# Performance work log

Measured on AMD Instinct MI355X. Metric: run time of the kernel, lower is better.

The kernel has to match this reference:

```python
import jax, jax.numpy as jnp
import numpy as np

N_NODES = 100000
N_EDGES = 1600000
D = 128


def _gconv(x, edge_index, edge_weight, W, Wloop, b):
    # support = x @ W ; out = adj @ support + x @ Wloop + b
    support = x @ W                                   # [N, D]
    src, dst = edge_index[0], edge_index[1]
    msgs = support[src] * edge_weight[:, None]        # [E, D] gather (irregular)
    agg = jax.ops.segment_sum(msgs, dst, num_segments=x.shape[0])  # [N, D] scatter
    return agg + x @ Wloop + b


def setup_inputs() -> dict:
    key = jax.random.key(0)
    ks = jax.random.split(key, 9)
    s = 1.0 / np.sqrt(D)
    x = jax.random.normal(ks[0], (N_NODES, D), dtype=jnp.float32)
    edge_index = jax.random.randint(ks[1], (2, N_EDGES), 0, N_NODES, dtype=jnp.int32)
    edge_weight = jax.random.uniform(ks[2], (N_EDGES,), dtype=jnp.float32)
    W1 = jax.random.normal(ks[3], (D, D), dtype=jnp.float32) * s
    Wloop1 = jax.random.normal(ks[4], (D, D), dtype=jnp.float32) * s
    b1 = jax.random.normal(ks[5], (D,), dtype=jnp.float32) * 0.01
    W2 = jax.random.normal(ks[6], (D, D), dtype=jnp.float32) * s
    Wloop2 = jax.random.normal(ks[7], (D, D), dtype=jnp.float32) * s
    b2 = jax.random.normal(ks[8], (D,), dtype=jnp.float32) * 0.01
    return {"x": x, "edge_index": edge_index, "edge_weight": edge_weight,
            "W1": W1, "Wloop1": Wloop1, "b1": b1,
            "W2": W2, "Wloop2": Wloop2, "b2": b2}


def reference(x, edge_index, edge_weight, W1, Wloop1, b1, W2, Wloop2, b2):
    h = _gconv(x, edge_index, edge_weight, W1, Wloop1, b1)
    h = _gconv(h, edge_index, edge_weight, W2, Wloop2, b2)
    return (x + h) * 0.5
```

## Files before the change

### kernel.cpp

```cpp
#include <hip/hip_runtime.h>
#include <hip/hip_bf16.h>
#include <stdint.h>

#define D 128
#define BM 64
#define NB_BITS 9
#define NPB (1 << NB_BITS)
#define BCAP 10240
#define C3_EPB 4096

typedef __attribute__((ext_vector_type(8))) short bf16x8;
typedef __attribute__((ext_vector_type(4))) short short4_t;
typedef __attribute__((ext_vector_type(4))) float f32x4;
typedef unsigned int uint32;

static __device__ __forceinline__ short f2bf(float f) {
  uint32_t u = __builtin_bit_cast(uint32_t, f);
  u += 0x7fffu + ((u >> 16) & 1u);
  return (short)(u >> 16);
}

static __device__ __forceinline__ uint32 pk2bf(float a, float b) {
  return ((uint32)(unsigned short)f2bf(b) << 16) | (uint32)(unsigned short)f2bf(a);
}


__global__ void k_prep(const float* __restrict__ W1, const float* __restrict__ Wl1,
                       const float* __restrict__ W2, const float* __restrict__ Wl2,
                       short* __restrict__ BT1, short* __restrict__ BT2,
                       int* __restrict__ bcur) {
  int idx = blockIdx.x * 256 + threadIdx.x;
  if (idx < 2 * D * D) {
    int n = idx >> 7, k = idx & (D - 1);
    float v = (n < D) ? W1[k * D + n] : Wl1[k * D + (n - D)];
    BT1[idx] = f2bf(v);
  } else if (idx < 4 * D * D) {
    int i2 = idx - 2 * D * D;
    int n = i2 >> 8, k = i2 & 255;
    float v = (k < D) ? W2[k * D + n] : Wl2[(k - D) * D + n];
    BT2[i2] = f2bf(v);
  } else if (idx < 4 * D * D + 256) {
    bcur[idx - 4 * D * D] = 0;
  }
}


__global__ __launch_bounds__(256) void k_bucket(const int* __restrict__ src,
                                                const int* __restrict__ dst,
                                                const float* __restrict__ wgt,
                                                int* __restrict__ bcur,
                                                int4* __restrict__ rec,
                                                int E, int nb) {
  __shared__ int lhist[256];
  __shared__ int lbase[256];
  const int t = threadIdx.x;
  const int e0 = blockIdx.x * C3_EPB;
  if (t < nb) lhist[t] = 0;
  __syncthreads();
  for (int i = t; i < C3_EPB; i += 256) {
    int e = e0 + i;
    if (e < E) atomicAdd(&lhist[dst[e] >> NB_BITS], 1);
  }
  __syncthreads();
  if (t < nb) {
    lbase[t] = atomicAdd(&bcur[t], lhist[t]);
    lhist[t] = 0;
  }
  __syncthreads();
  for (int i = t; i < C3_EPB; i += 256) {
    int e = e0 + i;
    if (e < E) {
      int d = dst[e];
      int b = d >> NB_BITS;
      int r = lbase[b] + atomicAdd(&lhist[b], 1);
      if (r >= BCAP) r = BCAP - 1;
      rec[(size_t)b * BCAP + r] =
          make_int4(src[e], __builtin_bit_cast(int, wgt[e]), d, 0);
    }
  }
}


__global__ __launch_bounds__(256) void k_sort(const int4* __restrict__ rec,
                                              const int* __restrict__ bcur,
                                              int* __restrict__ off,
                                              int2* __restrict__ pairs,
                                              int N, int nb) {
  __shared__ int bc[256];
  __shared__ int psum[256];
  __shared__ int lofs[NPB];
  const int t = threadIdx.x;
  const int b = blockIdx.x;

  int mycnt = (t < nb) ? min(bcur[t], BCAP) : 0;
  bc[t] = mycnt;
  __syncthreads();
  for (int dd = 1; dd < 256; dd <<= 1) {
    int a = (t >= dd) ? bc[t - dd] : 0;
    __syncthreads();
    bc[t] += a;
    __syncthreads();
  }
  const int cntb = min(bcur[b], BCAP);
  const int ebase = bc[b] - cntb;
  const int total = bc[nb - 1];
  const size_t rbase = (size_t)b * BCAP;
  const int n0 = b << NB_BITS;
  const int nn = min(NPB, N - n0);

  for (int i = t; i < NPB; i += 256) lofs[i] = 0;
  __syncthreads();
  for (int i = t; i < cntb; i += 256)
    atomicAdd(&lofs[rec[rbase + i].z & (NPB - 1)], 1);
  __syncthreads();

  int v0 = lofs[2 * t], v1 = lofs[2 * t + 1];
  int sum = v0 + v1;
  psum[t] = sum;
  __syncthreads();
  for (int dd = 1; dd < 256; dd <<= 1) {
    int a = (t >= dd) ? psum[t - dd] : 0;
    __syncthreads();
    psum[t] += a;
    __syncthreads();
  }
  int run = psum[t] - sum;
  lofs[2 * t] = run;
  lofs[2 * t + 1] = run + v0;
  __syncthreads();

  for (int i = t; i < nn; i += 256) off[n0 + i] = ebase + lofs[i];
  if (b == nb - 1 && t == 0) off[N] = total;
  __syncthreads();

  for (int i = t; i < cntb; i += 256) {
    int4 rr = rec[rbase + i];
    int r = atomicAdd(&lofs[rr.z & (NPB - 1)], 1);
    pairs[ebase + r] = make_int2(rr.x, rr.y);
  }
}


__global__ __launch_bounds__(256) void k_gemm1(const float* __restrict__ A,
                                               const short* __restrict__ BT,
                                               const float* __restrict__ bias,
                                               unsigned short* __restrict__ support,
                                               unsigned short* __restrict__ initp, int M) {
  __shared__ short As[BM * D];
  const int t = threadIdx.x;
  const int l = t & 63;
  const int w = t >> 6;
  const int lm = l & 15;
  const int lg = l >> 4;
  const int m0 = blockIdx.x * BM;
  const bool full = (m0 + BM <= M);

  float4 aregf[8];
#pragma unroll
  for (int i = 0; i < 8; ++i) {
    int id = t + i * 256;
    int row = id >> 5, c4 = id & 31;
    int gr = m0 + row; if (gr >= M) gr = M - 1;
    aregf[i] = *(const float4*)(A + (size_t)gr * D + c4 * 4);
  }

  bf16x8 bfrag[4][4];
  const int colbase = w * 64 + lm;
#pragma unroll
  for (int cf = 0; cf < 4; ++cf) {
    const short* p = BT + (colbase + cf * 16) * D + lg * 8;
#pragma unroll
    for (int ks = 0; ks < 4; ++ks) bfrag[cf][ks] = *(const bf16x8*)(p + ks * 32);
  }

#pragma unroll
  for (int i = 0; i < 8; ++i) {
    int id = t + i * 256;
    int row = id >> 5, c4 = id & 31;
    float4 v = aregf[i];
    short4_t s4 = { f2bf(v.x), f2bf(v.y), f2bf(v.z), f2bf(v.w) };
    int sidx = row * D + ((c4 * 4) ^ ((row & 7) << 3));
    *(short4_t*)(As + sidx) = s4;
  }
  __syncthreads();

  f32x4 acc[4][4] = {};
#pragma unroll
  for (int ks = 0; ks < 4; ++ks) {
    bf16x8 afrag[4];
    int kcol = ks * 32 + lg * 8;
#pragma unroll
    for (int rf = 0; rf < 4; ++rf) {
      int row = rf * 16 + lm;
      afrag[rf] = *(const bf16x8*)(As + row * D + (kcol ^ ((row & 7) << 3)));
    }
#pragma unroll
    for (int rf = 0; rf < 4; ++rf)
#pragma unroll
      for (int cf = 0; cf < 4; ++cf)
        acc[rf][cf] = __builtin_amdgcn_mfma_f32_16x16x32_bf16(
            bfrag[cf][ks], afrag[rf], acc[rf][cf], 0, 0, 0);
  }

  const bool isInit = (w >= 2);
  const int wcol = (w & 1) * 64;

  if (!isInit) {
#pragma unroll
    for (int rf = 0; rf < 4; ++rf) {
      int m = m0 + rf * 16 + lm;
#pragma unroll
      for (int cf = 0; cf < 4; ++cf) {
        int nb = wcol + cf * 16 + lg * 4;
        f32x4 a = acc[rf][cf];
        uint2 pk = make_uint2(pk2bf(a[0], a[1]), pk2bf(a[2], a[3]));
        if (full || m < M)
          *(uint2*)((uint32*)support + (size_t)m * 64 + (nb >> 1)) = pk;
      }
    }
  } else {
    float4 bv4[4];
#pragma unroll
    for (int cf = 0; cf < 4; ++cf)
      bv4[cf] = *(const float4*)(bias + wcol + cf * 16 + lg * 4);
#pragma unroll
    for (int rf = 0; rf < 4; ++rf) {
      int m = m0 + rf * 16 + lm;
      bool ok = full || m < M;
#pragma unroll
      for (int cf = 0; cf < 4; ++cf) {
        int nb = wcol + cf * 16 + lg * 4;
        f32x4 a = acc[rf][cf];
        if (ok) {
          uint2 pk = make_uint2(pk2bf(a[0] + bv4[cf].x, a[1] + bv4[cf].y),
                                pk2bf(a[2] + bv4[cf].z, a[3] + bv4[cf].w));
          *(uint2*)((uint32*)initp + (size_t)m * 64 + (nb >> 1)) = pk;
        }
      }
    }
  }
}


__global__ __launch_bounds__(256) void k_gemm2(const uint32* __restrict__ aggb,
                                               const uint32* __restrict__ h1b,
                                               const short* __restrict__ BT,
                                               const float* __restrict__ bias,
                                               const float* __restrict__ resid,
                                               float* __restrict__ out, int M) {
  __shared__ short As[BM * 256];
  const int t = threadIdx.x;
  const int l = t & 63;
  const int w = t >> 6;
  const int lm = l & 15;
  const int lg = l >> 4;
  const int m0 = blockIdx.x * BM;
  const bool full = (m0 + BM <= M);

#pragma unroll
  for (int i = 0; i < 8; ++i) {
    int id = t + i * 256;
    int row = id >> 5, c8 = id & 31;
    int gr = m0 + row; if (gr >= M) gr = M - 1;
    const uint32* srcp = (c8 < 16) ? (aggb + (size_t)gr * 64 + c8 * 4)
                                   : (h1b + (size_t)gr * 64 + (c8 - 16) * 4);
    uint4 v = *(const uint4*)srcp;
    int sidx = row * 256 + ((c8 * 8) ^ ((row & 7) << 3));
    *(uint4*)(As + sidx) = v;
  }

  bf16x8 bfrag[2][8];
  const int colbase = w * 32 + lm;
#pragma unroll
  for (int cf = 0; cf < 2; ++cf) {
    const short* p = BT + (colbase + cf * 16) * 256 + lg * 8;
#pragma unroll
    for (int ks = 0; ks < 8; ++ks) bfrag[cf][ks] = *(const bf16x8*)(p + ks * 32);
  }
  __syncthreads();

  f32x4 acc[4][2] = {};
#pragma unroll
  for (int ks = 0; ks < 8; ++ks) {
    bf16x8 afrag[4];
    int kcol = ks * 32 + lg * 8;
#pragma unroll
    for (int rf = 0; rf < 4; ++rf) {
      int row = rf * 16 + lm;
      afrag[rf] = *(const bf16x8*)(As + row * 256 + (kcol ^ ((row & 7) << 3)));
    }
#pragma unroll
    for (int rf = 0; rf < 4; ++rf)
#pragma unroll
      for (int cf = 0; cf < 2; ++cf)
        acc[rf][cf] = __builtin_amdgcn_mfma_f32_16x16x32_bf16(
            bfrag[cf][ks], afrag[rf], acc[rf][cf], 0, 0, 0);
  }

  float4 bv4[2];
#pragma unroll
  for (int cf = 0; cf < 2; ++cf)
    bv4[cf] = *(const float4*)(bias + w * 32 + cf * 16 + lg * 4);
#pragma unroll
  for (int rf = 0; rf < 4; ++rf) {
    int m = m0 + rf * 16 + lm;
    bool ok = full || m < M;
    if (!ok) continue;
#pragma unroll
    for (int cf = 0; cf < 2; ++cf) {
      int nb = w * 32 + cf * 16 + lg * 4;
      f32x4 a = acc[rf][cf];
      float4 xr = *(const float4*)(resid + (size_t)m * D + nb);
      float4 v;
      v.x = (a[0] + bv4[cf].x + xr.x) * 0.5f;
      v.y = (a[1] + bv4[cf].y + xr.y) * 0.5f;
      v.z = (a[2] + bv4[cf].z + xr.z) * 0.5f;
      v.w = (a[3] + bv4[cf].w + xr.w) * 0.5f;
      *(float4*)(out + (size_t)m * D + nb) = v;
    }
  }
}


template<int MODE>
__global__ __launch_bounds__(256) void k_agg(const uint32* __restrict__ sup,
                                             const int* __restrict__ off,
                                             const int2* __restrict__ pairs,
                                             uint32* __restrict__ iop, int N) {
  int node = blockIdx.x * 4 + (threadIdx.x >> 6);
  if (node >= N) return;
  const int l = threadIdx.x & 63;
  const int beg = __builtin_amdgcn_readfirstlane(off[node]);
  const int end = __builtin_amdgcn_readfirstlane(off[node + 1]);
  float ax = 0.f, ay = 0.f;
  const int nbt = (end - beg + 7) >> 3;

  if (nbt > 0) {
    int pr[8], pw[8];
#pragma unroll
    for (int i = 0; i < 8; ++i) {
      int jj = beg + i;
      int jc = jj < end ? jj : beg;
      int2 tt = pairs[jc];
      pr[i] = __builtin_amdgcn_readfirstlane(tt.x);
      pw[i] = __builtin_amdgcn_readfirstlane(jj < end ? tt.y : 0);
    }
    int j = beg + 8;
    for (int b = 1; b < nbt; ++b, j += 8) {
      int nr[8], nw[8];
#pragma unroll
      for (int i = 0; i < 8; ++i) {
        int jj = j + i;
        int jc = jj < end ? jj : beg;
        int2 tt = pairs[jc];
        nr[i] = __builtin_amdgcn_readfirstlane(tt.x);
        nw[i] = __builtin_amdgcn_readfirstlane(jj < end ? tt.y : 0);
      }
      uint32 v[8];
#pragma unroll
      for (int i = 0; i < 8; ++i) v[i] = sup[(size_t)(uint32)pr[i] * 64 + l];
#pragma unroll
      for (int i = 0; i < 8; ++i) {
        float w = __builtin_bit_cast(float, pw[i]);
        ax = fmaf(__builtin_bit_cast(float, v[i] << 16), w, ax);
        ay = fmaf(__builtin_bit_cast(float, v[i] & 0xffff0000u), w, ay);
      }
#pragma unroll
      for (int i = 0; i < 8; ++i) { pr[i] = nr[i]; pw[i] = nw[i]; }
    }
    uint32 v[8];
#pragma unroll
    for (int i = 0; i < 8; ++i) v[i] = sup[(size_t)(uint32)pr[i] * 64 + l];
#pragma unroll
    for (int i = 0; i < 8; ++i) {
      float w = __builtin_bit_cast(float, pw[i]);
      ax = fmaf(__builtin_bit_cast(float, v[i] << 16), w, ax);
      ay = fmaf(__builtin_bit_cast(float, v[i] & 0xffff0000u), w, ay);
    }
  }

  size_t o = (size_t)node * 64 + l;
  if (MODE == 0) {
    uint32 cur = iop[o];
    float vx = __builtin_bit_cast(float, cur << 16) + ax;
    float vy = __builtin_bit_cast(float, cur & 0xffff0000u) + ay;
    iop[o] = pk2bf(vx, vy);
  } else {
    iop[o] = pk2bf(ax, ay);
  }
}


extern "C" void kernel_launch(void* const* d_in, const int* in_sizes, int n_in,
                              void* d_out, int out_size, void* d_ws, size_t ws_size,
                              hipStream_t stream) {
  const float* x   = (const float*)d_in[0];
  const int*   ei  = (const int*)d_in[1];
  const float* ew  = (const float*)d_in[2];
  const float* W1  = (const float*)d_in[3];
  const float* Wl1 = (const float*)d_in[4];
  const float* b1  = (const float*)d_in[5];
  const float* W2  = (const float*)d_in[6];
  const float* Wl2 = (const float*)d_in[7];
  const float* b2  = (const float*)d_in[8];
  float* out = (float*)d_out;

  const int N = in_sizes[0] / D;
  const int E = in_sizes[1] / 2;
  const int* src = ei;
  const int* dst = ei + E;
  const int nbuck = (N + NPB - 1) >> NB_BITS;

  uint32* sup = (uint32*)d_ws;
  uint32* h1b = sup + (size_t)N * 64;
  short* BT1  = (short*)(h1b + (size_t)N * 64);
  short* BT2  = BT1 + 2 * D * D;
  int* bcur   = (int*)(BT2 + 2 * D * D);
  int* off    = bcur + 256;
  int2* pairs = (int2*)(off + (N + 4));
  int4* rec   = (int4*)(pairs + E);
  uint32* aggb = (uint32*)rec;

  k_prep<<<(4 * D * D + 256 + 255) / 256, 256, 0, stream>>>(W1, Wl1, W2, Wl2, BT1, BT2, bcur);

  k_bucket<<<(E + C3_EPB - 1) / C3_EPB, 256, 0, stream>>>(src, dst, ew, bcur, rec, E, nbuck);
  k_sort<<<nbuck, 256, 0, stream>>>(rec, bcur, off, pairs, N, nbuck);

  const int mblocks = (N + BM - 1) / BM;
  const int ablocks = (N + 3) / 4;

  k_gemm1<<<mblocks, 256, 0, stream>>>(x, BT1, b1, (unsigned short*)sup, (unsigned short*)h1b, N);
  k_agg<0><<<ablocks, 256, 0, stream>>>(sup, off, pairs, h1b, N);

  k_agg<2><<<ablocks, 256, 0, stream>>>(h1b, off, pairs, aggb, N);
  k_gemm2<<<mblocks, 256, 0, stream>>>(aggb, h1b, BT2, b2, x, out, N);
}
```

Measured before the change: 249.8 us.

## Fuse second-layer aggregation into the final GEMM kernel

The second gather/segment-sum is moved into the final GEMM kernel. Each wave aggregates 16 node rows into shared memory as bf16, and the h1 tile is loaded into a padded LDS buffer; the MFMA then reads both halves. This removes one kernel launch and the global write and re-read of the intermediate aggregate. In exchange, each block now aggregates its 64 rows with only 4 waves in sequence, so there is less parallelism to hide the latency of irregular gathers than in the separate 4-nodes-per-block kernel.

```diff
diff --git a/kernel.cpp b/kernel.cpp
--- a/kernel.cpp
+++ b/kernel.cpp
@@ -8,6 +8,7 @@
 #define NPB (1 << NB_BITS)
 #define BCAP 10240
 #define C3_EPB 4096
+#define LROW 136
 
 typedef __attribute__((ext_vector_type(8))) short bf16x8;
 typedef __attribute__((ext_vector_type(4))) short short4_t;
@@ -242,87 +243,6 @@
 }
 
 
-__global__ __launch_bounds__(256) void k_gemm2(const uint32* __restrict__ aggb,
-                                               const uint32* __restrict__ h1b,
-                                               const short* __restrict__ BT,
-                                               const float* __restrict__ bias,
-                                               const float* __restrict__ resid,
-                                               float* __restrict__ out, int M) {
-  __shared__ short As[BM * 256];
-  const int t = threadIdx.x;
-  const int l = t & 63;
-  const int w = t >> 6;
-  const int lm = l & 15;
-  const int lg = l >> 4;
-  const int m0 = blockIdx.x * BM;
-  const bool full = (m0 + BM <= M);
-
-#pragma unroll
-  for (int i = 0; i < 8; ++i) {
-    int id = t + i * 256;
-    int row = id >> 5, c8 = id & 31;
-    int gr = m0 + row; if (gr >= M) gr = M - 1;
-    const uint32* srcp = (c8 < 16) ? (aggb + (size_t)gr * 64 + c8 * 4)
-                                   : (h1b + (size_t)gr * 64 + (c8 - 16) * 4);
-    uint4 v = *(const uint4*)srcp;
-    int sidx = row * 256 + ((c8 * 8) ^ ((row & 7) << 3));
-    *(uint4*)(As + sidx) = v;
-  }
-
-  bf16x8 bfrag[2][8];
-  const int colbase = w * 32 + lm;
-#pragma unroll
-  for (int cf = 0; cf < 2; ++cf) {
-    const short* p = BT + (colbase + cf * 16) * 256 + lg * 8;
-#pragma unroll
-    for (int ks = 0; ks < 8; ++ks) bfrag[cf][ks] = *(const bf16x8*)(p + ks * 32);
-  }
-  __syncthreads();
-
-  f32x4 acc[4][2] = {};
-#pragma unroll
-  for (int ks = 0; ks < 8; ++ks) {
-    bf16x8 afrag[4];
-    int kcol = ks * 32 + lg * 8;
-#pragma unroll
-    for (int rf = 0; rf < 4; ++rf) {
-      int row = rf * 16 + lm;
-      afrag[rf] = *(const bf16x8*)(As + row * 256 + (kcol ^ ((row & 7) << 3)));
-    }
-#pragma unroll
-    for (int rf = 0; rf < 4; ++rf)
-#pragma unroll
-      for (int cf = 0; cf < 2; ++cf)
-        acc[rf][cf] = __builtin_amdgcn_mfma_f32_16x16x32_bf16(
-            bfrag[cf][ks], afrag[rf], acc[rf][cf], 0, 0, 0);
-  }
-
-  float4 bv4[2];
-#pragma unroll
-  for (int cf = 0; cf < 2; ++cf)
-    bv4[cf] = *(const float4*)(bias + w * 32 + cf * 16 + lg * 4);
-#pragma unroll
-  for (int rf = 0; rf < 4; ++rf) {
-    int m = m0 + rf * 16 + lm;
-    bool ok = full || m < M;
-    if (!ok) continue;
-#pragma unroll
-    for (int cf = 0; cf < 2; ++cf) {
-      int nb = w * 32 + cf * 16 + lg * 4;
-      f32x4 a = acc[rf][cf];
-      float4 xr = *(const float4*)(resid + (size_t)m * D + nb);
-      float4 v;
-      v.x = (a[0] + bv4[cf].x + xr.x) * 0.5f;
-      v.y = (a[1] + bv4[cf].y + xr.y) * 0.5f;
-      v.z = (a[2] + bv4[cf].z + xr.z) * 0.5f;
-      v.w = (a[3] + bv4[cf].w + xr.w) * 0.5f;
-      *(float4*)(out + (size_t)m * D + nb) = v;
-    }
-  }
-}
-
-
-template<int MODE>
 __global__ __launch_bounds__(256) void k_agg(const uint32* __restrict__ sup,
                                              const int* __restrict__ off,
                                              const int2* __restrict__ pairs,
@@ -380,13 +300,145 @@
   }
 
   size_t o = (size_t)node * 64 + l;
-  if (MODE == 0) {
-    uint32 cur = iop[o];
-    float vx = __builtin_bit_cast(float, cur << 16) + ax;
-    float vy = __builtin_bit_cast(float, cur & 0xffff0000u) + ay;
-    iop[o] = pk2bf(vx, vy);
-  } else {
-    iop[o] = pk2bf(ax, ay);
+  uint32 cur = iop[o];
+  float vx = __builtin_bit_cast(float, cur << 16) + ax;
+  float vy = __builtin_bit_cast(float, cur & 0xffff0000u) + ay;
+  iop[o] = pk2bf(vx, vy);
+}
+
+
+__global__ __launch_bounds__(256) void k_gemm2f(const uint32* __restrict__ h1b,
+                                                const short* __restrict__ BT,
+                                                const float* __restrict__ bias,
+                                                const float* __restrict__ resid,
+                                                const int* __restrict__ off,
+                                                const int2* __restrict__ pairs,
+                                                float* __restrict__ out, int M) {
+  __shared__ short Ag[BM * LROW];
+  __shared__ short Hh[BM * LROW];
+  const int t = threadIdx.x;
+  const int l = t & 63;
+  const int w = t >> 6;
+  const int lm = l & 15;
+  const int lg = l >> 4;
+  const int m0 = blockIdx.x * BM;
+  const bool full = (m0 + BM <= M);
+
+#pragma unroll
+  for (int i = 0; i < 4; ++i) {
+    int id = t + i * 256;
+    int row = id >> 4, c8 = id & 15;
+    int gr = m0 + row; if (gr >= M) gr = M - 1;
+    uint4 v = *(const uint4*)(h1b + (size_t)gr * 64 + c8 * 4);
+    *(uint4*)(Hh + row * LROW + c8 * 8) = v;
+  }
+
+  for (int r = 0; r < 16; ++r) {
+    const int row = w * 16 + r;
+    const int node = m0 + row;
+    float ax = 0.f, ay = 0.f;
+    if (node < M) {
+      const int beg = __builtin_amdgcn_readfirstlane(off[node]);
+      const int end = __builtin_amdgcn_readfirstlane(off[node + 1]);
+      const int nbt = (end - beg + 7) >> 3;
+      if (nbt > 0) {
+        int pr[8], pw[8];
+#pragma unroll
+        for (int i = 0; i < 8; ++i) {
+          int jj = beg + i;
+          int jc = jj < end ? jj : beg;
+          int2 tt = pairs[jc];
+          pr[i] = __builtin_amdgcn_readfirstlane(tt.x);
+          pw[i] = __builtin_amdgcn_readfirstlane(jj < end ? tt.y : 0);
+        }
+        int j = beg + 8;
+        for (int b = 1; b < nbt; ++b, j += 8) {
+          int nr[8], nw[8];
+#pragma unroll
+          for (int i = 0; i < 8; ++i) {
+            int jj = j + i;
+            int jc = jj < end ? jj : beg;
+            int2 tt = pairs[jc];
+            nr[i] = __builtin_amdgcn_readfirstlane(tt.x);
+            nw[i] = __builtin_amdgcn_readfirstlane(jj < end ? tt.y : 0);
+          }
+          uint32 v[8];
+#pragma unroll
+          for (int i = 0; i < 8; ++i) v[i] = h1b[(size_t)(uint32)pr[i] * 64 + l];
+#pragma unroll
+          for (int i = 0; i < 8; ++i) {
+            float wt = __builtin_bit_cast(float, pw[i]);
+            ax = fmaf(__builtin_bit_cast(float, v[i] << 16), wt, ax);
+            ay = fmaf(__builtin_bit_cast(float, v[i] & 0xffff0000u), wt, ay);
+          }
+#pragma unroll
+          for (int i = 0; i < 8; ++i) { pr[i] = nr[i]; pw[i] = nw[i]; }
+        }
+        uint32 v[8];
+#pragma unroll
+        for (int i = 0; i < 8; ++i) v[i] = h1b[(size_t)(uint32)pr[i] * 64 + l];
+#pragma unroll
+        for (int i = 0; i < 8; ++i) {
+          float wt = __builtin_bit_cast(float, pw[i]);
+          ax = fmaf(__builtin_bit_cast(float, v[i] << 16), wt, ax);
+          ay = fmaf(__builtin_bit_cast(float, v[i] & 0xffff0000u), wt, ay);
+        }
+      }
+    }
+    *(uint32*)(Ag + row * LROW + 2 * l) = pk2bf(ax, ay);
+  }
+  __syncthreads();
+
+  bf16x8 bfrag[2][8];
+  const int colbase = w * 32 + lm;
+#pragma unroll
+  for (int cf = 0; cf < 2; ++cf) {
+    const short* p = BT + (colbase + cf * 16) * 256 + lg * 8;
+#pragma unroll
+    for (int ks = 0; ks < 8; ++ks) bfrag[cf][ks] = *(const bf16x8*)(p + ks * 32);
+  }
+
+  f32x4 acc[4][2] = {};
+#pragma unroll
+  for (int ks = 0; ks < 8; ++ks) {
+    bf16x8 afrag[4];
+    int kcol = ks * 32 + lg * 8;
+#pragma unroll
+    for (int rf = 0; rf < 4; ++rf) {
+      int row = rf * 16 + lm;
+      afrag[rf] = (ks < 4)
+          ? *(const bf16x8*)(Ag + row * LROW + kcol)
+          : *(const bf16x8*)(Hh + row * LROW + (kcol - 128));
+    }
+#pragma unroll
+    for (int rf = 0; rf < 4; ++rf)
+#pragma unroll
+      for (int cf = 0; cf < 2; ++cf)
+        acc[rf][cf] = __builtin_amdgcn_mfma_f32_16x16x32_bf16(
+            bfrag[cf][ks], afrag[rf], acc[rf][cf], 0, 0, 0);
+  }
+
+  float4 bv4[2];
+#pragma unroll
+  for (int cf = 0; cf < 2; ++cf)
+    bv4[cf] = *(const float4*)(bias + w * 32 + cf * 16 + lg * 4);
+#pragma unroll
+  for (int rf = 0; rf < 4; ++rf) {
+    int m = m0 + rf * 16 + lm;
+    bool ok = full || m < M;
+    if (!ok) continue;
+#pragma unroll
+    for (int cf = 0; cf < 2; ++cf) {
+      int nb = w * 32 + cf * 16 + lg * 4;
+      f32x4 a = acc[rf][cf];
+      float4 xr = *(const float4*)(resid + (size_t)m * D + nb);
+      float4 v;
+      v.x = (a[0] + bv4[cf].x + xr.x) * 0.5f;
+      v.y = (a[1] + bv4[cf].y + xr.y) * 0.5f;
+      v.z = (a[2] + bv4[cf].z + xr.z) * 0.5f;
+      v.w = (a[3] + bv4[cf].w + xr.w) * 0.5f;
+      *(float4*)(out + (size_t)m * D + nb) = v;
+    }
   }
 }
 
@@ -419,7 +471,6 @@
   int* off    = bcur + 256;
   int2* pairs = (int2*)(off + (N + 4));
   int4* rec   = (int4*)(pairs + E);
-  uint32* aggb = (uint32*)rec;
 
   k_prep<<<(4 * D * D + 256 + 255) / 256, 256, 0, stream>>>(W1, Wl1, W2, Wl2, BT1, BT2, bcur);
 
@@ -430,8 +481,7 @@
   const int ablocks = (N + 3) / 4;
 
   k_gemm1<<<mblocks, 256, 0, stream>>>(x, BT1, b1, (unsigned short*)sup, (unsigned short*)h1b, N);
-  k_agg<0><<<ablocks, 256, 0, stream>>>(sup, off, pairs, h1b, N);
-
-  k_agg<2><<<ablocks, 256, 0, stream>>>(h1b, off, pairs, aggb, N);
-  k_gemm2<<<mblocks, 256, 0, stream>>>(aggb, h1b, BT2, b2, x, out, N);
-}
+  k_agg<<<ablocks, 256, 0, stream>>>(sup, off, pairs, h1b, N);
+
+  k_gemm2f<<<mblocks, 256, 0, stream>>>(h1b, BT2, b2, x, off, pairs, out, N);
+}
```

New measurement: 270.7 us. 1.08x slower.

## Merge edge bucketing and first GEMM into one heterogeneous launch

Applied to the files above, without the earlier changes.

Bucketing of edges and the first dense GEMM were two separate launches. They are now one kernel: block indices below bblocks do the bucketing and the rest do GEMM tiles, sharing a raw shared-memory buffer. This removes a launch and the serialisation between two independent stages, so the memory-bound bucketing and the compute-bound GEMM can overlap on the GPU. k_sort now runs after the combined kernel, and the aggregation kernel definition moves earlier in the file. The cost is that bucketing blocks reserve the GEMM-sized shared allocation, which may limit occupancy.

```diff
diff --git a/kernel.cpp b/kernel.cpp
--- a/kernel.cpp
+++ b/kernel.cpp
@@ -45,37 +45,140 @@
 }
 
 
-__global__ __launch_bounds__(256) void k_bucket(const int* __restrict__ src,
-                                                const int* __restrict__ dst,
-                                                const float* __restrict__ wgt,
-                                                int* __restrict__ bcur,
-                                                int4* __restrict__ rec,
-                                                int E, int nb) {
-  __shared__ int lhist[256];
-  __shared__ int lbase[256];
+__global__ __launch_bounds__(256) void k_b1(const int* __restrict__ src,
+                                            const int* __restrict__ dst,
+                                            const float* __restrict__ wgt,
+                                            int* __restrict__ bcur,
+                                            int4* __restrict__ rec,
+                                            int E, int nb, int bblocks,
+                                            const float* __restrict__ A,
+                                            const short* __restrict__ BT,
+                                            const float* __restrict__ bias,
+                                            unsigned short* __restrict__ support,
+                                            unsigned short* __restrict__ initp, int M) {
+  __shared__ char smraw[BM * D * 2];
   const int t = threadIdx.x;
-  const int e0 = blockIdx.x * C3_EPB;
-  if (t < nb) lhist[t] = 0;
-  __syncthreads();
-  for (int i = t; i < C3_EPB; i += 256) {
-    int e = e0 + i;
-    if (e < E) atomicAdd(&lhist[dst[e] >> NB_BITS], 1);
-  }
-  __syncthreads();
-  if (t < nb) {
-    lbase[t] = atomicAdd(&bcur[t], lhist[t]);
-    lhist[t] = 0;
-  }
-  __syncthreads();
-  for (int i = t; i < C3_EPB; i += 256) {
-    int e = e0 + i;
-    if (e < E) {
-      int d = dst[e];
-      int b = d >> NB_BITS;
-      int r = lbase[b] + atomicAdd(&lhist[b], 1);
-      if (r >= BCAP) r = BCAP - 1;
-      rec[(size_t)b * BCAP + r] =
-          make_int4(src[e], __builtin_bit_cast(int, wgt[e]), d, 0);
+
+  if (blockIdx.x < bblocks) {
+    int* lhist = (int*)smraw;
+    int* lbase = lhist + 256;
+    const int e0 = blockIdx.x * C3_EPB;
+    if (t < nb) lhist[t] = 0;
+    __syncthreads();
+    for (int i = t; i < C3_EPB; i += 256) {
+      int e = e0 + i;
+      if (e < E) atomicAdd(&lhist[dst[e] >> NB_BITS], 1);
+    }
+    __syncthreads();
+    if (t < nb) {
+      lbase[t] = atomicAdd(&bcur[t], lhist[t]);
+      lhist[t] = 0;
+    }
+    __syncthreads();
+    for (int i = t; i < C3_EPB; i += 256) {
+      int e = e0 + i;
+      if (e < E) {
+        int d = dst[e];
+        int b = d >> NB_BITS;
+        int r = lbase[b] + atomicAdd(&lhist[b], 1);
+        if (r >= BCAP) r = BCAP - 1;
+        rec[(size_t)b * BCAP + r] =
+            make_int4(src[e], __builtin_bit_cast(int, wgt[e]), d, 0);
+      }
+    }
+    return;
+  }
+
+  short* As = (short*)smraw;
+  const int l = t & 63;
+  const int w = t >> 6;
+  const int lm = l & 15;
+  const int lg = l >> 4;
+  const int m0 = (blockIdx.x - bblocks) * BM;
+  const bool full = (m0 + BM <= M);
+
+  float4 aregf[8];
+#pragma unroll
+  for (int i = 0; i < 8; ++i) {
+    int id = t + i * 256;
+    int row = id >> 5, c4 = id & 31;
+    int gr = m0 + row; if (gr >= M) gr = M - 1;
+    aregf[i] = *(const float4*)(A + (size_t)gr * D + c4 * 4);
+  }
+
+  bf16x8 bfrag[4][4];
+  const int colbase = w * 64 + lm;
+#pragma unroll
+  for (int cf = 0; cf < 4; ++cf) {
+    const short* p = BT + (colbase + cf * 16) * D + lg * 8;
+#pragma unroll
+    for (int ks = 0; ks < 4; ++ks) bfrag[cf][ks] = *(const bf16x8*)(p + ks * 32);
+  }
+
+#pragma unroll
+  for (int i = 0; i < 8; ++i) {
+    int id = t + i * 256;
+    int row = id >> 5, c4 = id & 31;
+    float4 v = aregf[i];
+    short4_t s4 = { f2bf(v.x), f2bf(v.y), f2bf(v.z), f2bf(v.w) };
+    int sidx = row * D + ((c4 * 4) ^ ((row & 7) << 3));
+    *(short4_t*)(As + sidx) = s4;
+  }
+  __syncthreads();
+
+  f32x4 acc[4][4] = {};
+#pragma unroll
+  for (int ks = 0; ks < 4; ++ks) {
+    bf16x8 afrag[4];
+    int kcol = ks * 32 + lg * 8;
+#pragma unroll
+    for (int rf = 0; rf < 4; ++rf) {
+      int row = rf * 16 + lm;
+      afrag[rf] = *(const bf16x8*)(As + row * D + (kcol ^ ((row & 7) << 3)));
+    }
+#pragma unroll
+    for (int rf = 0; rf < 4; ++rf)
+#pragma unroll
+      for (int cf = 0; cf < 4; ++cf)
+        acc[rf][cf] = __builtin_amdgcn_mfma_f32_16x16x32_bf16(
+            bfrag[cf][ks], afrag[rf], acc[rf][cf], 0, 0, 0);
+  }
+
+  const bool isInit = (w >= 2);
+  const int wcol = (w & 1) * 64;
+
+  if (!isInit) {
+#pragma unroll
+    for (int rf = 0; rf < 4; ++rf) {
+      int m = m0 + rf * 16 + lm;
+#pragma unroll
+      for (int cf = 0; cf < 4; ++cf) {
+        int nb2 = wcol + cf * 16 + lg * 4;
+        f32x4 a = acc[rf][cf];
+        uint2 pk = make_uint2(pk2bf(a[0], a[1]), pk2bf(a[2], a[3]));
+        if (full || m < M)
+          *(uint2*)((uint32*)support + (size_t)m * 64 + (nb2 >> 1)) = pk;
+      }
+    }
+  } else {
+    float4 bv4[4];
+#pragma unroll
+    for (int cf = 0; cf < 4; ++cf)
+      bv4[cf] = *(const float4*)(bias + wcol + cf * 16 + lg * 4);
+#pragma unroll
+    for (int rf = 0; rf < 4; ++rf) {
+      int m = m0 + rf * 16 + lm;
+      bool ok = full || m < M;
+#pragma unroll
+      for (int cf = 0; cf < 4; ++cf) {
+        int nb2 = wcol + cf * 16 + lg * 4;
+        f32x4 a = acc[rf][cf];
+        if (ok) {
+          uint2 pk = make_uint2(pk2bf(a[0] + bv4[cf].x, a[1] + bv4[cf].y),
+                                pk2bf(a[2] + bv4[cf].z, a[3] + bv4[cf].w));
+          *(uint2*)((uint32*)initp + (size_t)m * 64 + (nb2 >> 1)) = pk;
+        }
+      }
     }
   }
 }
@@ -141,103 +244,71 @@
 }
 
 
-__global__ __launch_bounds__(256) void k_gemm1(const float* __restrict__ A,
-                                               const short* __restrict__ BT,
-                                               const float* __restrict__ bias,
-                                               unsigned short* __restrict__ support,
-                                               unsigned short* __restrict__ initp, int M) {
-  __shared__ short As[BM * D];
-  const int t = threadIdx.x;
-  const int l = t & 63;
-  const int w = t >> 6;
-  const int lm = l & 15;
-  const int lg = l >> 4;
-  const int m0 = blockIdx.x * BM;
-  const bool full = (m0 + BM <= M);
-
-  float4 aregf[8];
-#pragma unroll
-  for (int i = 0; i < 8; ++i) {
-    int id = t + i * 256;
-    int row = id >> 5, c4 = id & 31;
-    int gr = m0 + row; if (gr >= M) gr = M - 1;
-    aregf[i] = *(const float4*)(A + (size_t)gr * D + c4 * 4);
-  }
-
-  bf16x8 bfrag[4][4];
-  const int colbase = w * 64 + lm;
-#pragma unroll
-  for (int cf = 0; cf < 4; ++cf) {
-    const short* p = BT + (colbase + cf * 16) * D + lg * 8;
-#pragma unroll
-    for (int ks = 0; ks < 4; ++ks) bfrag[cf][ks] = *(const bf16x8*)(p + ks * 32);
-  }
-
-#pragma unroll
-  for (int i = 0; i < 8; ++i) {
-    int id = t + i * 256;
-    int row = id >> 5, c4 = id & 31;
-    float4 v = aregf[i];
-    short4_t s4 = { f2bf(v.x), f2bf(v.y), f2bf(v.z), f2bf(v.w) };
-    int sidx = row * D + ((c4 * 4) ^ ((row & 7) << 3));
-    *(short4_t*)(As + sidx) = s4;
-  }
-  __syncthreads();
-
-  f32x4 acc[4][4] = {};
-#pragma unroll
-  for (int ks = 0; ks < 4; ++ks) {
-    bf16x8 afrag[4];
-    int kcol = ks * 32 + lg * 8;
-#pragma unroll
-    for (int rf = 0; rf < 4; ++rf) {
-      int row = rf * 16 + lm;
-      afrag[rf] = *(const bf16x8*)(As + row * D + (kcol ^ ((row & 7) << 3)));
-    }
-#pragma unroll
-    for (int rf = 0; rf < 4; ++rf)
-#pragma unroll
-      for (int cf = 0; cf < 4; ++cf)
-        acc[rf][cf] = __builtin_amdgcn_mfma_f32_16x16x32_bf16(
-            bfrag[cf][ks], afrag[rf], acc[rf][cf], 0, 0, 0);
-  }
-
-  const bool isInit = (w >= 2);
-  const int wcol = (w & 1) * 64;
-
-  if (!isInit) {
-#pragma unroll
-    for (int rf = 0; rf < 4; ++rf) {
-      int m = m0 + rf * 16 + lm;
-#pragma unroll
-      for (int cf = 0; cf < 4; ++cf) {
-        int nb = wcol + cf * 16 + lg * 4;
-        f32x4 a = acc[rf][cf];
-        uint2 pk = make_uint2(pk2bf(a[0], a[1]), pk2bf(a[2], a[3]));
-        if (full || m < M)
-          *(uint2*)((uint32*)support + (size_t)m * 64 + (nb >> 1)) = pk;
+template<int MODE>
+__global__ __launch_bounds__(256) void k_agg(const uint32* __restrict__ sup,
+                                             const int* __restrict__ off,
+                                             const int2* __restrict__ pairs,
+                                             uint32* __restrict__ iop, int N) {
+  int node = blockIdx.x * 4 + (threadIdx.x >> 6);
+  if (node >= N) return;
+  const int l = threadIdx.x & 63;
+  const int beg = __builtin_amdgcn_readfirstlane(off[node]);
+  const int end = __builtin_amdgcn_readfirstlane(off[node + 1]);
+  float ax = 0.f, ay = 0.f;
+  const int nbt = (end - beg + 7) >> 3;
+
+  if (nbt > 0) {
+    int pr[8], pw[8];
+#pragma unroll
+    for (int i = 0; i < 8; ++i) {
+      int jj = beg + i;
+      int jc = jj < end ? jj : beg;
+      int2 tt = pairs[jc];
+      pr[i] = __builtin_amdgcn_readfirstlane(tt.x);
+      pw[i] = __builtin_amdgcn_readfirstlane(jj < end ? tt.y : 0);
+    }
+    int j = beg + 8;
+    for (int b = 1; b < nbt; ++b, j += 8) {
+      int nr[8], nw[8];
+#pragma unroll
+      for (int i = 0; i < 8; ++i) {
+        int jj = j + i;
+        int jc = jj < end ? jj : beg;
+        int2 tt = pairs[jc];
+        nr[i] = __builtin_amdgcn_readfirstlane(tt.x);
+        nw[i] = __builtin_amdgcn_readfirstlane(jj < end ? tt.y : 0);
       }
-    }
+      uint32 v[8];
+#pragma unroll
+      for (int i = 0; i < 8; ++i) v[i] = sup[(size_t)(uint32)pr[i] * 64 + l];
+#pragma unroll
+      for (int i = 0; i < 8; ++i) {
+        float w = __builtin_bit_cast(float, pw[i]);
+        ax = fmaf(__builtin_bit_cast(float, v[i] << 16), w, ax);
+        ay = fmaf(__builtin_bit_cast(float, v[i] & 0xffff0000u), w, ay);
+      }
+#pragma unroll
+      for (int i = 0; i < 8; ++i) { pr[i] = nr[i]; pw[i] = nw[i]; }
+    }
+    uint32 v[8];
+#pragma unroll
+    for (int i = 0; i < 8; ++i) v[i] = sup[(size_t)(uint32)pr[i] * 64 + l];
+#pragma unroll
+    for (int i = 0; i < 8; ++i) {
+      float w = __builtin_bit_cast(float, pw[i]);
+      ax = fmaf(__builtin_bit_cast(float, v[i] << 16), w, ax);
+      ay = fmaf(__builtin_bit_cast(float, v[i] & 0xffff0000u), w, ay);
+    }
+  }
+
+  size_t o = (size_t)node * 64 + l;
+  if (MODE == 0) {
+    uint32 cur = iop[o];
+    float vx = __builtin_bit_cast(float, cur << 16) + ax;
+    float vy = __builtin_bit_cast(float, cur & 0xffff0000u) + ay;
+    iop[o] = pk2bf(vx, vy);
   } else {
-    float4 bv4[4];
-#pragma unroll
-    for (int cf = 0; cf < 4; ++cf)
-      bv4[cf] = *(const float4*)(bias + wcol + cf * 16 + lg * 4);
-#pragma unroll
-    for (int rf = 0; rf < 4; ++rf) {
-      int m = m0 + rf * 16 + lm;
-      bool ok = full || m < M;
-#pragma unroll
-      for (int cf = 0; cf < 4; ++cf) {
-        int nb = wcol + cf * 16 + lg * 4;
-        f32x4 a = acc[rf][cf];
-        if (ok) {
-          uint2 pk = make_uint2(pk2bf(a[0] + bv4[cf].x, a[1] + bv4[cf].y),
-                                pk2bf(a[2] + bv4[cf].z, a[3] + bv4[cf].w));
-          *(uint2*)((uint32*)initp + (size_t)m * 64 + (nb >> 1)) = pk;
-        }
-      }
-    }
+    iop[o] = pk2bf(ax, ay);
   }
 }
 
@@ -322,75 +393,6 @@
 }
 
 
-template<int MODE>
-__global__ __launch_bounds__(256) void k_agg(const uint32* __restrict__ sup,
-                                             const int* __restrict__ off,
-                                             const int2* __restrict__ pairs,
-                                             uint32* __restrict__ iop, int N) {
-  int node = blockIdx.x * 4 + (threadIdx.x >> 6);
-  if (node >= N) return;
-  const int l = threadIdx.x & 63;
-  const int beg = __builtin_amdgcn_readfirstlane(off[node]);
-  const int end = __builtin_amdgcn_readfirstlane(off[node + 1]);
-  float ax = 0.f, ay = 0.f;
-  const int nbt = (end - beg + 7) >> 3;
-
-  if (nbt > 0) {
-    int pr[8], pw[8];
-#pragma unroll
-    for (int i = 0; i < 8; ++i) {
-      int jj = beg + i;
-      int jc = jj < end ? jj : beg;
-      int2 tt = pairs[jc];
-      pr[i] = __builtin_amdgcn_readfirstlane(tt.x);
-      pw[i] = __builtin_amdgcn_readfirstlane(jj < end ? tt.y : 0);
-    }
-    int j = beg + 8;
-    for (int b = 1; b < nbt; ++b, j += 8) {
-      int nr[8], nw[8];
-#pragma unroll
-      for (int i = 0; i < 8; ++i) {
-        int jj = j + i;
-        int jc = jj < end ? jj : beg;
-        int2 tt = pairs[jc];
-        nr[i] = __builtin_amdgcn_readfirstlane(tt.x);
-        nw[i] = __builtin_amdgcn_readfirstlane(jj < end ? tt.y : 0);
-      }
-      uint32 v[8];
-#pragma unroll
-      for (int i = 0; i < 8; ++i) v[i] = sup[(size_t)(uint32)pr[i] * 64 + l];
-#pragma unroll
-      for (int i = 0; i < 8; ++i) {
-        float w = __builtin_bit_cast(float, pw[i]);
-        ax = fmaf(__builtin_bit_cast(float, v[i] << 16), w, ax);
-        ay = fmaf(__builtin_bit_cast(float, v[i] & 0xffff0000u), w, ay);
-      }
-#pragma unroll
-      for (int i = 0; i < 8; ++i) { pr[i] = nr[i]; pw[i] = nw[i]; }
-    }
-    uint32 v[8];
-#pragma unroll
-    for (int i = 0; i < 8; ++i) v[i] = sup[(size_t)(uint32)pr[i] * 64 + l];
-#pragma unroll
-    for (int i = 0; i < 8; ++i) {
-      float w = __builtin_bit_cast(float, pw[i]);
-      ax = fmaf(__builtin_bit_cast(float, v[i] << 16), w, ax);
-      ay = fmaf(__builtin_bit_cast(float, v[i] & 0xffff0000u), w, ay);
-    }
-  }
-
-  size_t o = (size_t)node * 64 + l;
-  if (MODE == 0) {
-    uint32 cur = iop[o];
-    float vx = __builtin_bit_cast(float, cur << 16) + ax;
-    float vy = __builtin_bit_cast(float, cur & 0xffff0000u) + ay;
-    iop[o] = pk2bf(vx, vy);
-  } else {
-    iop[o] = pk2bf(ax, ay);
-  }
-}
-
-
 extern "C" void kernel_launch(void* const* d_in, const int* in_sizes, int n_in,
                               void* d_out, int out_size, void* d_ws, size_t ws_size,
                               hipStream_t stream) {
@@ -423,13 +425,16 @@
 
   k_prep<<<(4 * D * D + 256 + 255) / 256, 256, 0, stream>>>(W1, Wl1, W2, Wl2, BT1, BT2, bcur);
 
-  k_bucket<<<(E + C3_EPB - 1) / C3_EPB, 256, 0, stream>>>(src, dst, ew, bcur, rec, E, nbuck);
-  k_sort<<<nbuck, 256, 0, stream>>>(rec, bcur, off, pairs, N, nbuck);
-
+  const int bblocks = (E + C3_EPB - 1) / C3_EPB;
   const int mblocks = (N + BM - 1) / BM;
   const int ablocks = (N + 3) / 4;
 
-  k_gemm1<<<mblocks, 256, 0, stream>>>(x, BT1, b1, (unsigned short*)sup, (unsigned short*)h1b, N);
+  k_b1<<<bblocks + mblocks, 256, 0, stream>>>(src, dst, ew, bcur, rec, E, nbuck, bblocks,
+                                              x, BT1, b1,
+                                              (unsigned short*)sup, (unsigned short*)h1b, N);
+
+  k_sort<<<nbuck, 256, 0, stream>>>(rec, bcur, off, pairs, N, nbuck);
+
   k_agg<0><<<ablocks, 256, 0, stream>>>(sup, off, pairs, h1b, N);
 
   k_agg<2><<<ablocks, 256, 0, stream>>>(h1b, off, pairs, aggb, N);
```

After: 237.0 us. -5.1%, faster.
